# Performance work log

Measured on AMD Instinct MI355X. Metric: run time of the kernel, lower is better.

The kernel has to match this reference:

```python
import jax, jax.numpy as jnp
import numpy as np

DISTANCE_EPS = 0.1


def setup_inputs() -> dict:
    key = jax.random.key(0)
    k1, k2, k3 = jax.random.split(key, 3)
    B, N, K, A = 2, 2048, 48, 4
    X = jax.random.normal(k1, (B, N, A, 3), dtype=jnp.float32)
    edge_idx = jax.random.randint(k2, (B, N, K), 0, N)
    C = jax.random.randint(k3, (B, N), 0, 4)
    return {"X": X, "edge_idx": edge_idx, "C": C}


def _normed_vec(V, eps=DISTANCE_EPS):
    # normalize with smoothing eps added to squared magnitude
    return V / jnp.sqrt((V * V).sum(-1, keepdims=True) + eps)


def reference(X, edge_idx, C):
    B, N, K = edge_idx.shape
    A = X.shape[2]
    X_flat = X.reshape(B, N, A * 3)
    batch = jnp.arange(B)[:, None, None]

    # Edge2mers: gather neighbor coords and concat with self coords
    X_j = X_flat[batch, edge_idx]                                   # (B,N,K,3A)
    X_i = jnp.broadcast_to(X_flat[:, :, None, :], (B, N, K, A * 3))  # (B,N,K,3A)
    X_ij = jnp.concatenate([X_i, X_j], -1).reshape(B, N, K, 2 * A, 3)

    mask_i = (C > 0).astype(jnp.float32)[..., None]   # (B,N,1)
    mask_j = mask_i[batch, edge_idx]                  # (B,N,K,1)
    mask_ij = mask_i[:, :, None, :] * mask_j          # (B,N,K,1)

    # pairwise normalized difference vectors: [a,b] = X_ij[b] - X_ij[a]
    U_ij = _normed_vec(X_ij[:, :, :, None, :, :] - X_ij[:, :, :, :, None, :])  # (B,N,K,2A,2A,3)

    # per-residue backbone frame from N, CA, C atoms
    X_N, X_CA, X_Cc = X[:, :, 0], X[:, :, 1], X[:, :, 2]
    u_CA_N = _normed_vec(X_N - X_CA)
    u_CA_C = _normed_vec(X_Cc - X_CA)
    n_1 = u_CA_N
    n_2 = _normed_vec(jnp.cross(n_1, u_CA_C))
    n_3 = _normed_vec(jnp.cross(n_1, n_2))
    R = jnp.stack([n_1, n_2, n_3], -1)  # (B,N,3,3)

    # rotate each pairwise vector into the local frame of residue i
    U_rot = jnp.einsum('nijabx,nixy->nijaby', U_ij, R)
    feature_ij = U_rot.reshape(B, N, K, -1)           # (B,N,K,3*(2A)^2)
    edge_h = mask_ij * feature_ij
    return edge_h
```

## Files before the change

### kernel.cpp

```cpp
#include <hip/hip_runtime.h>


constexpr int Bq = 2, Nq = 2048, Kq = 48;
constexpr float EPS = 0.1f;

typedef float vf4 __attribute__((ext_vector_type(4)));

struct F3 { float x, y, z; };
__device__ __forceinline__ F3 f3sub(F3 a, F3 b) { return {a.x - b.x, a.y - b.y, a.z - b.z}; }
__device__ __forceinline__ float f3dot(F3 a, F3 b) {
    return fmaf(a.x, b.x, fmaf(a.y, b.y, a.z * b.z));
}
__device__ __forceinline__ F3 f3scale(F3 a, float s) { return {a.x * s, a.y * s, a.z * s}; }
__device__ __forceinline__ F3 f3normed(F3 v) {
    float inv = rsqrtf(f3dot(v, v) + EPS);
    return f3scale(v, inv);
}
__device__ __forceinline__ F3 f3cross(F3 a, F3 b) {
    return {a.y * b.z - a.z * b.y, a.z * b.x - a.x * b.z, a.x * b.y - a.y * b.x};
}

__global__ __launch_bounds__(256) void edge_orient_v4_kernel(
    const float* __restrict__ X,
    const int* __restrict__ E,
    const int* __restrict__ C,
    float* __restrict__ out)
{
    __shared__ vf4 smem[768];

    const int t = threadIdx.x;
    const unsigned edge = blockIdx.x * 16u + (unsigned)(t >> 4);
    const unsigned sub  = t & 15u;
    const unsigned a    = sub >> 1;
    const unsigned half = sub & 1u;

    const unsigned node = edge / (unsigned)Kq;
    const unsigned bidx = node >> 11;
    const int j = E[edge];
    const unsigned nodej = (bidx << 11) + (unsigned)j;

    const float m = (C[node] > 0 && C[nodej] > 0) ? 1.0f : 0.0f;

    const vf4* Xi4 = reinterpret_cast<const vf4*>(X + (size_t)node * 12);
    const vf4* Xj4 = reinterpret_cast<const vf4*>(X + (size_t)nodej * 12);
    const vf4 A0 = Xi4[0], A1 = Xi4[1], A2 = Xi4[2];

    const F3 p0 = {A0.x, A0.y, A0.z};
    const F3 p1 = {A0.w, A1.x, A1.y};
    const F3 p2 = {A1.z, A1.w, A2.x};
    const F3 n1u = f3normed(f3sub(p0, p1));
    const F3 uC  = f3normed(f3sub(p2, p1));
    const F3 n2u = f3normed(f3cross(n1u, uC));
    const F3 n3u = f3normed(f3cross(n1u, n2u));
    const F3 n1 = f3scale(n1u, m), n2 = f3scale(n2u, m), n3 = f3scale(n3u, m);

    const vf4* Pb4 = half ? Xj4 : Xi4;
    const vf4 Q0 = Pb4[0], Q1 = Pb4[1], Q2 = Pb4[2];
    const F3 q0 = {Q0.x, Q0.y, Q0.z};
    const F3 q1 = {Q0.w, Q1.x, Q1.y};
    const F3 q2 = {Q1.z, Q1.w, Q2.x};
    const F3 q3 = {Q2.y, Q2.z, Q2.w};

    const float* pap = X + (size_t)(a < 4u ? node : nodej) * 12 + (a & 3u) * 3;
    const F3 pa = {pap[0], pap[1], pap[2]};

    float o[12] __attribute__((aligned(16)));
#pragma unroll
    for (int k = 0; k < 4; ++k) {
        F3 pb;
        switch (k) {
            case 0: pb = q0; break; case 1: pb = q1; break;
            case 2: pb = q2; break; default: pb = q3; break;
        }
        const F3 d = f3sub(pb, pa);
        const float nn = fmaf(d.x, d.x, fmaf(d.y, d.y, fmaf(d.z, d.z, EPS)));
        const float inv = rsqrtf(nn);
        o[k * 3 + 0] = f3dot(d, n1) * inv;
        o[k * 3 + 1] = f3dot(d, n2) * inv;
        o[k * 3 + 2] = f3dot(d, n3) * inv;
    }

    const vf4* ov = reinterpret_cast<const vf4*>(o);
#pragma unroll
    for (int i = 0; i < 3; ++i) smem[3 * t + i] = ov[i];
    __syncthreads();

    vf4* outb = reinterpret_cast<vf4*>(out) + (size_t)blockIdx.x * 768;
#pragma unroll
    for (int s = 0; s < 3; ++s) {
        const int g = s * 256 + t;
        __builtin_nontemporal_store(smem[g], &outb[g]);
    }
}

extern "C" void kernel_launch(void* const* d_in, const int* in_sizes, int n_in,
                              void* d_out, int out_size, void* d_ws, size_t ws_size,
                              hipStream_t stream) {
    const float* X = (const float*)d_in[0];
    const int*   E = (const int*)d_in[1];
    const int*   C = (const int*)d_in[2];
    float* out = (float*)d_out;

    const int total_edges = Bq * Nq * Kq;
    dim3 block(256);
    dim3 grid(total_edges / 16);
    edge_orient_v4_kernel<<<grid, block, 0, stream>>>(X, E, C, out);
}
```

Baseline: 29.72 us.

## Process four edge groups per wave with wave-local smem staging instead of block barrier

Each block now covers 64 edges instead of 16. Each wave loops over four groups of 4 edges and stages its results in its own double-buffered shared-memory region. The block-wide __syncthreads is replaced by a wave barrier plus an lgkmcnt wait, so waves transpose and store their output independently. This removes block-level synchronisation and cuts the block count, in exchange for less parallelism per launch and serial work within each wave.

Result: slower. 35.21 us (+18.5%).

```diff
diff --git a/kernel.cpp b/kernel.cpp
--- a/kernel.cpp
+++ b/kernel.cpp
@@ -20,76 +20,92 @@
     return {a.y * b.z - a.z * b.y, a.z * b.x - a.x * b.z, a.x * b.y - a.y * b.x};
 }
 
-__global__ __launch_bounds__(256) void edge_orient_v4_kernel(
+__global__ __launch_bounds__(256) void edge_orient_v6_kernel(
     const float* __restrict__ X,
     const int* __restrict__ E,
     const int* __restrict__ C,
     float* __restrict__ out)
 {
-    __shared__ vf4 smem[768];
+    __shared__ vf4 smem[1536];
 
     const int t = threadIdx.x;
-    const unsigned edge = blockIdx.x * 16u + (unsigned)(t >> 4);
-    const unsigned sub  = t & 15u;
+    const int w = t >> 6;
+    const int l = t & 63;
+    vf4* const wbase = smem + w * 384;
+
+    const unsigned sub  = (unsigned)l & 15u;
     const unsigned a    = sub >> 1;
     const unsigned half = sub & 1u;
 
-    const unsigned node = edge / (unsigned)Kq;
-    const unsigned bidx = node >> 11;
-    const int j = E[edge];
-    const unsigned nodej = (bidx << 11) + (unsigned)j;
+    const unsigned ewave = blockIdx.x * 64u + (unsigned)w * 16u;
+    vf4* const f4out = reinterpret_cast<vf4*>(out);
 
-    const float m = (C[node] > 0 && C[nodej] > 0) ? 1.0f : 0.0f;
+#pragma unroll
+    for (int g = 0; g < 4; ++g) {
+        const unsigned egrp = ewave + (unsigned)g * 4u;
+        const unsigned edge = egrp + ((unsigned)l >> 4);
 
-    const vf4* Xi4 = reinterpret_cast<const vf4*>(X + (size_t)node * 12);
-    const vf4* Xj4 = reinterpret_cast<const vf4*>(X + (size_t)nodej * 12);
-    const vf4 A0 = Xi4[0], A1 = Xi4[1], A2 = Xi4[2];
+        const unsigned node = edge / (unsigned)Kq;
+        const unsigned bidx = node >> 11;
+        const int j = E[edge];
+        const unsigned nodej = (bidx << 11) + (unsigned)j;
 
-    const F3 p0 = {A0.x, A0.y, A0.z};
-    const F3 p1 = {A0.w, A1.x, A1.y};
-    const F3 p2 = {A1.z, A1.w, A2.x};
-    const F3 n1u = f3normed(f3sub(p0, p1));
-    const F3 uC  = f3normed(f3sub(p2, p1));
-    const F3 n2u = f3normed(f3cross(n1u, uC));
-    const F3 n3u = f3normed(f3cross(n1u, n2u));
-    const F3 n1 = f3scale(n1u, m), n2 = f3scale(n2u, m), n3 = f3scale(n3u, m);
+        const float m = (C[node] > 0 && C[nodej] > 0) ? 1.0f : 0.0f;
 
-    const vf4* Pb4 = half ? Xj4 : Xi4;
-    const vf4 Q0 = Pb4[0], Q1 = Pb4[1], Q2 = Pb4[2];
-    const F3 q0 = {Q0.x, Q0.y, Q0.z};
-    const F3 q1 = {Q0.w, Q1.x, Q1.y};
-    const F3 q2 = {Q1.z, Q1.w, Q2.x};
-    const F3 q3 = {Q2.y, Q2.z, Q2.w};
+        const vf4* Xi4 = reinterpret_cast<const vf4*>(X + (size_t)node * 12);
+        const vf4* Xj4 = reinterpret_cast<const vf4*>(X + (size_t)nodej * 12);
+        const vf4 A0 = Xi4[0], A1 = Xi4[1], A2 = Xi4[2];
 
-    const float* pap = X + (size_t)(a < 4u ? node : nodej) * 12 + (a & 3u) * 3;
-    const F3 pa = {pap[0], pap[1], pap[2]};
+        const F3 p0 = {A0.x, A0.y, A0.z};
+        const F3 p1 = {A0.w, A1.x, A1.y};
+        const F3 p2 = {A1.z, A1.w, A2.x};
+        const F3 n1u = f3normed(f3sub(p0, p1));
+        const F3 uC  = f3normed(f3sub(p2, p1));
+        const F3 n2u = f3normed(f3cross(n1u, uC));
+        const F3 n3u = f3normed(f3cross(n1u, n2u));
+        const F3 n1 = f3scale(n1u, m), n2 = f3scale(n2u, m), n3 = f3scale(n3u, m);
 
-    float o[12] __attribute__((aligned(16)));
+        const vf4* Pb4 = half ? Xj4 : Xi4;
+        const vf4 Q0 = Pb4[0], Q1 = Pb4[1], Q2 = Pb4[2];
+        const F3 q0 = {Q0.x, Q0.y, Q0.z};
+        const F3 q1 = {Q0.w, Q1.x, Q1.y};
+        const F3 q2 = {Q1.z, Q1.w, Q2.x};
+        const F3 q3 = {Q2.y, Q2.z, Q2.w};
+
+        const float* pap = X + (size_t)(a < 4u ? node : nodej) * 12 + (a & 3u) * 3;
+        const F3 pa = {pap[0], pap[1], pap[2]};
+
+        float o[12] __attribute__((aligned(16)));
 #pragma unroll
-    for (int k = 0; k < 4; ++k) {
-        F3 pb;
-        switch (k) {
-            case 0: pb = q0; break; case 1: pb = q1; break;
-            case 2: pb = q2; break; default: pb = q3; break;
+        for (int k = 0; k < 4; ++k) {
+            F3 pb;
+            switch (k) {
+                case 0: pb = q0; break; case 1: pb = q1; break;
+                case 2: pb = q2; break; default: pb = q3; break;
+            }
+            const F3 d = f3sub(pb, pa);
+            const float nn = fmaf(d.x, d.x, fmaf(d.y, d.y, fmaf(d.z, d.z, EPS)));
+            const float inv = rsqrtf(nn);
+            o[k * 3 + 0] = f3dot(d, n1) * inv;
+            o[k * 3 + 1] = f3dot(d, n2) * inv;
+            o[k * 3 + 2] = f3dot(d, n3) * inv;
         }
-        const F3 d = f3sub(pb, pa);
-        const float nn = fmaf(d.x, d.x, fmaf(d.y, d.y, fmaf(d.z, d.z, EPS)));
-        const float inv = rsqrtf(nn);
-        o[k * 3 + 0] = f3dot(d, n1) * inv;
-        o[k * 3 + 1] = f3dot(d, n2) * inv;
-        o[k * 3 + 2] = f3dot(d, n3) * inv;
-    }
 
-    const vf4* ov = reinterpret_cast<const vf4*>(o);
+        vf4* const ws = wbase + (g & 1) * 192;
+        const vf4* ov = reinterpret_cast<const vf4*>(o);
 #pragma unroll
-    for (int i = 0; i < 3; ++i) smem[3 * t + i] = ov[i];
-    __syncthreads();
+        for (int i = 0; i < 3; ++i) ws[3 * l + i] = ov[i];
 
-    vf4* outb = reinterpret_cast<vf4*>(out) + (size_t)blockIdx.x * 768;
+        __builtin_amdgcn_wave_barrier();
+        asm volatile("s_waitcnt lgkmcnt(0)" ::: "memory");
+        __builtin_amdgcn_sched_barrier(0);
+
+        vf4* outg = f4out + (size_t)egrp * 48;
 #pragma unroll
-    for (int s = 0; s < 3; ++s) {
-        const int g = s * 256 + t;
-        __builtin_nontemporal_store(smem[g], &outb[g]);
+        for (int s = 0; s < 3; ++s) {
+            const int gidx = s * 64 + l;
+            __builtin_nontemporal_store(ws[gidx], &outg[gidx]);
+        }
     }
 }
 
@@ -103,6 +119,6 @@
 
     const int total_edges = Bq * Nq * Kq;
     dim3 block(256);
-    dim3 grid(total_edges / 16);
-    edge_orient_v4_kernel<<<grid, block, 0, stream>>>(X, E, C, out);
+    dim3 grid(total_edges / 64);
+    edge_orient_v6_kernel<<<grid, block, 0, stream>>>(X, E, C, out);
 }
```

## Process six edge tiles per block with double-buffered LDS and prefetched indices

Applied to the files above, without the earlier changes.

Each block now loops over six 16-edge tiles instead of handling one, which cuts the grid size by six. LDS is double-buffered so one tile's stores can overlap the next tile's compute with a single barrier per tile. The next tile's edge index is prefetched after the barrier. Output stores switch from nontemporal to regular stores, which changes cache behaviour for the write-heavy output and gives less parallelism across blocks.

Result: slower. 32.39 us (+9.0%).

```diff
diff --git a/kernel.cpp b/kernel.cpp
--- a/kernel.cpp
+++ b/kernel.cpp
@@ -2,6 +2,7 @@
 
 
 constexpr int Bq = 2, Nq = 2048, Kq = 48;
+constexpr int TILES = 6, TILE_EDGES = 16;
 constexpr float EPS = 0.1f;
 
 typedef float vf4 __attribute__((ext_vector_type(4)));
@@ -20,76 +21,90 @@
     return {a.y * b.z - a.z * b.y, a.z * b.x - a.x * b.z, a.x * b.y - a.y * b.x};
 }
 
-__global__ __launch_bounds__(256) void edge_orient_v4_kernel(
+__global__ __launch_bounds__(256) void edge_orient_v7_kernel(
     const float* __restrict__ X,
     const int* __restrict__ E,
     const int* __restrict__ C,
     float* __restrict__ out)
 {
-    __shared__ vf4 smem[768];
+    __shared__ vf4 smem[1536];
 
     const int t = threadIdx.x;
-    const unsigned edge = blockIdx.x * 16u + (unsigned)(t >> 4);
-    const unsigned sub  = t & 15u;
+    const unsigned sub  = (unsigned)t & 15u;
     const unsigned a    = sub >> 1;
     const unsigned half = sub & 1u;
 
-    const unsigned node = edge / (unsigned)Kq;
-    const unsigned bidx = node >> 11;
-    const int j = E[edge];
-    const unsigned nodej = (bidx << 11) + (unsigned)j;
+    const unsigned eblock = blockIdx.x * (unsigned)(TILES * TILE_EDGES);
+    const unsigned erow   = (unsigned)(t >> 4);
+    vf4* const f4out = reinterpret_cast<vf4*>(out);
 
-    const float m = (C[node] > 0 && C[nodej] > 0) ? 1.0f : 0.0f;
+    int jreg = E[eblock + erow];
 
-    const vf4* Xi4 = reinterpret_cast<const vf4*>(X + (size_t)node * 12);
-    const vf4* Xj4 = reinterpret_cast<const vf4*>(X + (size_t)nodej * 12);
-    const vf4 A0 = Xi4[0], A1 = Xi4[1], A2 = Xi4[2];
+#pragma unroll 2
+    for (int g = 0; g < TILES; ++g) {
+        const unsigned etile = eblock + (unsigned)g * TILE_EDGES;
+        const unsigned edge  = etile + erow;
 
-    const F3 p0 = {A0.x, A0.y, A0.z};
-    const F3 p1 = {A0.w, A1.x, A1.y};
-    const F3 p2 = {A1.z, A1.w, A2.x};
-    const F3 n1u = f3normed(f3sub(p0, p1));
-    const F3 uC  = f3normed(f3sub(p2, p1));
-    const F3 n2u = f3normed(f3cross(n1u, uC));
-    const F3 n3u = f3normed(f3cross(n1u, n2u));
-    const F3 n1 = f3scale(n1u, m), n2 = f3scale(n2u, m), n3 = f3scale(n3u, m);
+        const unsigned node = edge / (unsigned)Kq;
+        const unsigned bidx = node >> 11;
+        const unsigned nodej = (bidx << 11) + (unsigned)jreg;
 
-    const vf4* Pb4 = half ? Xj4 : Xi4;
-    const vf4 Q0 = Pb4[0], Q1 = Pb4[1], Q2 = Pb4[2];
-    const F3 q0 = {Q0.x, Q0.y, Q0.z};
-    const F3 q1 = {Q0.w, Q1.x, Q1.y};
-    const F3 q2 = {Q1.z, Q1.w, Q2.x};
-    const F3 q3 = {Q2.y, Q2.z, Q2.w};
+        const float m = (C[node] > 0 && C[nodej] > 0) ? 1.0f : 0.0f;
 
-    const float* pap = X + (size_t)(a < 4u ? node : nodej) * 12 + (a & 3u) * 3;
-    const F3 pa = {pap[0], pap[1], pap[2]};
+        const vf4* Xi4 = reinterpret_cast<const vf4*>(X + (size_t)node * 12);
+        const vf4* Xj4 = reinterpret_cast<const vf4*>(X + (size_t)nodej * 12);
+        const vf4 A0 = Xi4[0], A1 = Xi4[1], A2 = Xi4[2];
 
-    float o[12] __attribute__((aligned(16)));
+        const F3 p0 = {A0.x, A0.y, A0.z};
+        const F3 p1 = {A0.w, A1.x, A1.y};
+        const F3 p2 = {A1.z, A1.w, A2.x};
+        const F3 n1u = f3normed(f3sub(p0, p1));
+        const F3 uC  = f3normed(f3sub(p2, p1));
+        const F3 n2u = f3normed(f3cross(n1u, uC));
+        const F3 n3u = f3normed(f3cross(n1u, n2u));
+        const F3 n1 = f3scale(n1u, m), n2 = f3scale(n2u, m), n3 = f3scale(n3u, m);
+
+        const vf4* Pb4 = half ? Xj4 : Xi4;
+        const vf4 Q0 = Pb4[0], Q1 = Pb4[1], Q2 = Pb4[2];
+        const F3 q0 = {Q0.x, Q0.y, Q0.z};
+        const F3 q1 = {Q0.w, Q1.x, Q1.y};
+        const F3 q2 = {Q1.z, Q1.w, Q2.x};
+        const F3 q3 = {Q2.y, Q2.z, Q2.w};
+
+        const float* pap = X + (size_t)(a < 4u ? node : nodej) * 12 + (a & 3u) * 3;
+        const F3 pa = {pap[0], pap[1], pap[2]};
+
+        float o[12] __attribute__((aligned(16)));
 #pragma unroll
-    for (int k = 0; k < 4; ++k) {
-        F3 pb;
-        switch (k) {
-            case 0: pb = q0; break; case 1: pb = q1; break;
-            case 2: pb = q2; break; default: pb = q3; break;
+        for (int k = 0; k < 4; ++k) {
+            F3 pb;
+            switch (k) {
+                case 0: pb = q0; break; case 1: pb = q1; break;
+                case 2: pb = q2; break; default: pb = q3; break;
+            }
+            const F3 d = f3sub(pb, pa);
+            const float nn = fmaf(d.x, d.x, fmaf(d.y, d.y, fmaf(d.z, d.z, EPS)));
+            const float inv = rsqrtf(nn);
+            o[k * 3 + 0] = f3dot(d, n1) * inv;
+            o[k * 3 + 1] = f3dot(d, n2) * inv;
+            o[k * 3 + 2] = f3dot(d, n3) * inv;
         }
-        const F3 d = f3sub(pb, pa);
-        const float nn = fmaf(d.x, d.x, fmaf(d.y, d.y, fmaf(d.z, d.z, EPS)));
-        const float inv = rsqrtf(nn);
-        o[k * 3 + 0] = f3dot(d, n1) * inv;
-        o[k * 3 + 1] = f3dot(d, n2) * inv;
-        o[k * 3 + 2] = f3dot(d, n3) * inv;
-    }
 
-    const vf4* ov = reinterpret_cast<const vf4*>(o);
+        vf4* const buf = smem + (g & 1) * 768;
+        const vf4* ov = reinterpret_cast<const vf4*>(o);
 #pragma unroll
-    for (int i = 0; i < 3; ++i) smem[3 * t + i] = ov[i];
-    __syncthreads();
+        for (int i = 0; i < 3; ++i) buf[3 * t + i] = ov[i];
 
-    vf4* outb = reinterpret_cast<vf4*>(out) + (size_t)blockIdx.x * 768;
+        __syncthreads();
+
+        if (g + 1 < TILES) jreg = E[etile + TILE_EDGES + erow];
+
+        vf4* outb = f4out + (size_t)etile * 48;
 #pragma unroll
-    for (int s = 0; s < 3; ++s) {
-        const int g = s * 256 + t;
-        __builtin_nontemporal_store(smem[g], &outb[g]);
+        for (int s = 0; s < 3; ++s) {
+            const int gi = s * 256 + t;
+            outb[gi] = buf[gi];
+        }
     }
 }
 
@@ -103,6 +118,6 @@
 
     const int total_edges = Bq * Nq * Kq;
     dim3 block(256);
-    dim3 grid(total_edges / 16);
-    edge_orient_v4_kernel<<<grid, block, 0, stream>>>(X, E, C, out);
+    dim3 grid(total_edges / (TILES * TILE_EDGES));
+    edge_orient_v7_kernel<<<grid, block, 0, stream>>>(X, E, C, out);
 }
```
